# Kernel tuning notes

Measured on AMD Instinct MI355X. Metric: run time of the kernel, lower is better.

## Reference

```python
import jax, jax.numpy as jnp
import numpy as np

B, C, H = 4, 256, 8
GRID = 64                  # 64x64 quads, 2 triangles each
F = 2 * GRID * GRID        # 8192 faces
D = C // H
N_STEPS = 4 * GRID + 8     # upper bound on BFS wavefronts over the face graph


def _grid_adjacency():
    """Face adjacency (<=3 neighbors, -1 padded) of a triangulated GRIDxGRID quad grid."""
    adj = -np.ones((F, 3), np.int32)
    qid = lambda r, c: 2 * (r * GRID + c)
    for r in range(GRID):
        for c in range(GRID):
            t0 = qid(r, c); t1 = t0 + 1
            n0, n1 = [t1], [t0]
            if c > 0:        n0.append(qid(r, c - 1) + 1)
            if r > 0:        n0.append(qid(r - 1, c) + 1)
            if c < GRID - 1: n1.append(qid(r, c + 1))
            if r < GRID - 1: n1.append(qid(r + 1, c))
            adj[t0, :len(n0)] = n0
            adj[t1, :len(n1)] = n1
    return adj


def setup_inputs() -> dict:
    key = jax.random.key(0)
    k1, k2, k3, k4 = jax.random.split(key, 4)
    x = jax.random.normal(k1, (B, C, F), jnp.float32)
    Wq = jax.random.normal(k2, (C, C), jnp.float32) / np.sqrt(C).astype(np.float32)
    Wk = jax.random.normal(k3, (C, C), jnp.float32) / np.sqrt(C).astype(np.float32)
    adj = jnp.tile(jnp.asarray(_grid_adjacency())[None], (B, 1, 1))
    anchors = jax.random.randint(k4, (B,), 0, F, jnp.int32)
    return {"x": x, "Wq": Wq, "Wk": Wk, "adj": adj, "anchors": anchors}


def _heads(W, x):
    """Project and L2-normalize per head: [B,C,F] -> [B,H,D,F] unit vectors along D."""
    y = jnp.einsum('oc,bcf->bof', W, x).reshape(x.shape[0], H, D, -1)
    return y * jax.lax.rsqrt(jnp.sum(y * y, axis=2, keepdims=True) + 1e-12)


def reference(x, Wq, Wk, adj, anchors):
    q = _heads(Wq, x)          # [B,H,D,F]
    k = _heads(Wk, x)          # [B,H,D,F]
    bidx = jnp.arange(B)

    # initial scores: normalized attention map between all faces and the anchor face,
    # mapped to [0,1] and averaged over heads  (atnmap+1)/2 path of the torch module
    k_anchor = k[bidx, :, :, anchors]                       # [B,H,D]
    cos0 = jnp.einsum('bhdf,bhd->bhf', q, k_anchor)         # [B,H,F]
    scores0 = (jnp.mean(cos0, axis=1) + 1.0) * 0.5          # [B,F]

    ktot = k.sum(axis=3)                                    # [B,H,D]
    valid = adj >= 0
    adj_s = jnp.where(valid, adj, 0)
    done0 = jnp.zeros((B, F), bool).at[bidx, anchors].set(True)
    boundary0 = done0

    def gather(v):  # v: [B,F] -> neighbor values [B,F,3]
        return jnp.take_along_axis(v, adj_s.reshape(B, -1), axis=1).reshape(B, F, 3)

    def step(carry, _):
        done, boundary, scores = carry
        bf = boundary.astype(x.dtype)
        nb = bf.sum(1)                       # |boundary|
        no = F - nb                          # |others| = complement of boundary
        # mean over (heads, boundary, others) of cosine(q_b, k_o):
        # mean_{b,o} q_b.k_o = (sum_b q_b).(sum_o k_o) / (nb*no)
        qs = jnp.einsum('bhdf,bf->bhd', q, bf)
        ko = ktot - jnp.einsum('bhdf,bf->bhd', k, bf)
        mean_cos = jnp.einsum('bhd,bhd->b', qs, ko) / (H * jnp.maximum(nb * no, 1.0))
        pred = (mean_cos + 1.0) * 0.5        # scalar per mesh, as in torch reshape(1,-1).mean
        # neighbor score: max score among already-visited (done) adjacent faces, else 1
        n_done = gather(done) & valid
        n_sc = gather(scores)
        neigh = jnp.where(jnp.any(n_done, -1),
                          jnp.max(jnp.where(n_done, n_sc, -jnp.inf), -1), 1.0)
        cand = jnp.minimum(jnp.maximum(pred[:, None], scores), neigh)
        scores = jnp.where(boundary, cand, scores)
        done = done | boundary
        boundary = jnp.any(gather(boundary) & valid, -1) & ~done
        return (done, boundary, scores), None

    (_, _, scores), _ = jax.lax.scan(jax.checkpoint(step),
                                     (done0, boundary0, scores0), None, length=N_STEPS)
    # with atn_layers=1 the torch module never modifies features: final_features == x
    return x, scores
```

## Files before the change

### kernel.cpp

```cpp
#include <hip/hip_runtime.h>
#include <hip/hip_bf16.h>
#include <stdint.h>

#define B_ 4
#define C_ 256
#define H_ 8
#define F_ 8192
#define NSTEPS_ 264
#define OC_ 512

typedef __attribute__((ext_vector_type(8))) short short8;
typedef __attribute__((ext_vector_type(4))) float f32x4;

static __device__ __forceinline__ unsigned f2bf(float f) {
  unsigned u = __float_as_uint(f);
  return (u + 0x7FFFu + ((u >> 16) & 1u)) >> 16;
}
static __device__ __forceinline__ float b2f(unsigned short s) {
  return __uint_as_float(((unsigned)s) << 16);
}

static __device__ __forceinline__ void face_neighbors(int f, int nn[3]) {
  int qd = f >> 1, r = qd >> 6, c = qd & 63;
  if ((f & 1) == 0) {
    nn[0] = f + 1;
    nn[1] = (c > 0) ? f - 1 : -1;
    nn[2] = (r > 0) ? f - 127 : -1;
  } else {
    nn[0] = f - 1;
    nn[1] = (c < 63) ? f + 1 : -1;
    nn[2] = (r < 63) ? f + 127 : -1;
  }
}

static __device__ __forceinline__ int face_dist(int ra, int ca, int pa, int f) {
  int qd = f >> 1, r = qd >> 6, c = qd & 63, p = f & 1;
  int dr = r - ra, dc = c - ca;
  int I = max(dr, 0) + max(dc, 0);
  int D = max(-dr, 0) + max(-dc, 0);
  int lo = pa ? max(2 * I - 1, 2 * D) : max(2 * I, 2 * D - 1);
  lo = max(lo, 0);
  lo += (lo ^ p ^ pa) & 1;
  return lo;
}

__global__ void k_pre(const float* __restrict__ Wq, const float* __restrict__ Wk,
                      uint16_t* __restrict__ Wbf) {
  const int gid = blockIdx.x * 256 + threadIdx.x;
  const int base = gid * 32;
  const float* src = (base < 65536) ? (Wq + base) : (Wk + (base - 65536));
  uint32_t pk[16];
#pragma unroll
  for (int j = 0; j < 16; ++j) {
    float2 v = *(const float2*)(src + j * 2);
    pk[j] = f2bf(v.x) | (f2bf(v.y) << 16);
  }
  uint4* dst = (uint4*)(Wbf + base);
#pragma unroll
  for (int s = 0; s < 4; ++s)
    dst[s] = make_uint4(pk[4 * s], pk[4 * s + 1], pk[4 * s + 2], pk[4 * s + 3]);
}

__launch_bounds__(256)
__global__ void k_gemm(const float* __restrict__ x, const uint16_t* __restrict__ Wbf,
                       uint16_t* __restrict__ qkT, const int* __restrict__ anchors,
                       uint16_t* __restrict__ order_g, uint32_t* __restrict__ lvlOff_g,
                       uint32_t* __restrict__ chunks_g, uint32_t* __restrict__ nch_g,
                       float* __restrict__ ktot) {
  __shared__ char smem[65536];
  char* Xl = smem;
  char* Wl0 = smem + 32768;
  char* Wl1 = smem + 49152;
  const int tid = threadIdx.x;
  const int b = blockIdx.z;

  if (blockIdx.x == 128) {
    uint8_t* dLv = (uint8_t*)smem;
    uint16_t* ordL = (uint16_t*)(smem + 8192);
    uint32_t* hist = (uint32_t*)(smem + 24576);
    uint32_t* loff = (uint32_t*)(smem + 25600);
    uint32_t* cnt = (uint32_t*)(smem + 26640);
    uint32_t* chOff = (uint32_t*)(smem + 27680);
    const int a = anchors[b];
    const int aq = a >> 1, ra = aq >> 6, ca = aq & 63, pa = a & 1;
    hist[tid] = 0; cnt[tid] = 0;
    __syncthreads();
#pragma unroll
    for (int j = 0; j < 32; ++j) {
      int f = j * 256 + tid;
      int d = face_dist(ra, ca, pa, f);
      dLv[f] = (uint8_t)d;
      atomicAdd(&hist[d], 1u);
    }
    __syncthreads();
    loff[tid + 1] = hist[tid];
    if (tid == 0) loff[0] = 0;
    __syncthreads();
    for (int ofs = 1; ofs < 256; ofs <<= 1) {
      uint32_t v = (tid >= ofs) ? loff[tid + 1 - ofs] : 0u;
      __syncthreads();
      loff[tid + 1] += v;
      __syncthreads();
    }
#pragma unroll
    for (int j = 0; j < 32; ++j) {
      int f = j * 256 + tid;
      int d = dLv[f];
      int nn[3];
      face_neighbors(f, nn);
      int mask = 0;
      if (nn[0] >= 0 && dLv[nn[0]] < d) mask |= 1;
      if (nn[1] >= 0 && dLv[nn[1]] < d) mask |= 2;
      if (nn[2] >= 0 && dLv[nn[2]] < d) mask |= 4;
      uint32_t pos = loff[d] + atomicAdd(&cnt[d], 1u);
      ordL[pos] = (uint16_t)(f | (mask << 13));
    }
    __syncthreads();
    for (int i = tid; i < F_; i += 256) order_g[b * F_ + i] = ordL[i];
    for (int l = tid; l < NSTEPS_ + 2; l += 256)
      lvlOff_g[b * (NSTEPS_ + 2) + l] = (l <= 256) ? loff[l] : (uint32_t)F_;
    const int n_l = (int)(loff[tid + 1] - loff[tid]);
    const int chc = (n_l + 63) >> 6;
    chOff[tid + 1] = (uint32_t)chc;
    if (tid == 0) chOff[0] = 0;
    __syncthreads();
    for (int ofs = 1; ofs < 256; ofs <<= 1) {
      uint32_t v = (tid >= ofs) ? chOff[tid + 1 - ofs] : 0u;
      __syncthreads();
      chOff[tid + 1] += v;
      __syncthreads();
    }
    const uint32_t cbase = chOff[tid];
    for (int j = 0; j < chc; ++j) {
      uint32_t cs = loff[tid] + (uint32_t)(j * 64);
      uint32_t cl = (uint32_t)min(64, n_l - j * 64);
      chunks_g[b * 512 + cbase + j] = cs | (cl << 16);
    }
    if (tid == 255) nch_g[b] = chOff[256];
    return;
  }

  const int f0 = blockIdx.x * 64;
  const int lane = tid & 63;
  const int wo = tid >> 6;
  const int lq = lane >> 4;
  const int lm = lane & 15;

  {
    const int fx = tid & 63;
    const int kseg = tid >> 6;
    const float* src = x + ((size_t)b * C_ + kseg * 64) * F_ + f0 + fx;
#pragma unroll
    for (int g = 0; g < 4; ++g) {
      uint32_t pk[8];
#pragma unroll
      for (int j2 = 0; j2 < 8; ++j2) {
        float v0 = src[(size_t)(g * 16 + 2 * j2) * F_];
        float v1 = src[(size_t)(g * 16 + 2 * j2 + 1) * F_];
        pk[j2] = f2bf(v0) | (f2bf(v1) << 16);
      }
#pragma unroll
      for (int s = 0; s < 2; ++s) {
        int slot = kseg * 8 + g * 2 + s;
        uint32_t* dst = (uint32_t*)(Xl + (size_t)fx * 512 + ((slot ^ (fx & 7)) << 4));
        dst[0] = pk[4 * s + 0]; dst[1] = pk[4 * s + 1];
        dst[2] = pk[4 * s + 2]; dst[3] = pk[4 * s + 3];
      }
    }
  }

  for (int p = 0; p < 4; ++p) {
    const int o0 = p * 128;
    const uint16_t* Wsrc = Wbf + (size_t)o0 * C_;
#pragma unroll
    for (int j = 0; j < 4; ++j) {
      int sl = tid * 4 + j;
      int ocl = sl >> 3, slot = sl & 7;
      uint4 v = *(const uint4*)(Wsrc + (size_t)ocl * C_ + slot * 8);
      *(uint4*)(Wl0 + (size_t)ocl * 128 + ((slot ^ (ocl & 7)) << 4)) = v;
    }
    __syncthreads();

    f32x4 acc[4][2] = {};
    for (int kt = 0; kt < 4; ++kt) {
      char* cur = (kt & 1) ? Wl1 : Wl0;
      char* nxt = (kt & 1) ? Wl0 : Wl1;
      uint4 wv[4];
      if (kt < 3) {
#pragma unroll
        for (int j = 0; j < 4; ++j) {
          int sl = tid * 4 + j;
          int ocl = sl >> 3, slot = sl & 7;
          wv[j] = *(const uint4*)(Wsrc + (size_t)ocl * C_ + (kt + 1) * 64 + slot * 8);
        }
      }
#pragma unroll
      for (int kk = 0; kk < 64; kk += 32) {
        const int sA = kt * 8 + (kk >> 3) + lq;
        const int sB = (kk >> 3) + lq;
        short8 af[4], bg[2];
#pragma unroll
        for (int mi = 0; mi < 4; ++mi) {
          int fl = mi * 16 + lm;
          af[mi] = *(const short8*)(Xl + (size_t)fl * 512 + ((sA ^ (fl & 7)) << 4));
        }
#pragma unroll
        for (int ni = 0; ni < 2; ++ni) {
          int ocl = wo * 32 + ni * 16 + lm;
          bg[ni] = *(const short8*)(cur + (size_t)ocl * 128 + ((sB ^ (ocl & 7)) << 4));
        }
#pragma unroll
        for (int mi = 0; mi < 4; ++mi)
#pragma unroll
          for (int ni = 0; ni < 2; ++ni)
            acc[mi][ni] = __builtin_amdgcn_mfma_f32_16x16x32_bf16(af[mi], bg[ni], acc[mi][ni], 0, 0, 0);
      }
      if (kt < 3) {
#pragma unroll
        for (int j = 0; j < 4; ++j) {
          int sl = tid * 4 + j;
          int ocl = sl >> 3, slot = sl & 7;
          *(uint4*)(nxt + (size_t)ocl * 128 + ((slot ^ (ocl & 7)) << 4)) = wv[j];
        }
      }
      __syncthreads();
    }

    char* yst = Wl0;
#pragma unroll
    for (int mi = 0; mi < 4; ++mi) {
#pragma unroll
      for (int r = 0; r < 4; ++r) {
        float s0 = acc[mi][0][r] * acc[mi][0][r] + acc[mi][1][r] * acc[mi][1][r];
        s0 += __shfl_xor(s0, 1);
        s0 += __shfl_xor(s0, 2);
        s0 += __shfl_xor(s0, 4);
        s0 += __shfl_xor(s0, 8);
        const float sc0 = rsqrtf(s0 + 1e-12f);
        const int fl = mi * 16 + lq * 4 + r;
#pragma unroll
        for (int ni = 0; ni < 2; ++ni) {
          int ocl = wo * 32 + ni * 16 + lm;
          float v = acc[mi][ni][r] * sc0;
          int byte = fl * 256 + ((((ocl * 2) >> 4) ^ (fl & 7)) << 4) + ((ocl * 2) & 15);
          *(uint16_t*)(yst + byte) = (uint16_t)f2bf(v);
        }
      }
    }
    __syncthreads();
    uint32_t* qk32 = (uint32_t*)qkT;
    const size_t obase = (((size_t)b * F_ + f0) * OC_ + o0) >> 1;
    for (int idx = tid; idx < 4096; idx += 256) {
      int face = idx >> 6, wd = idx & 63;
      int byte = face * 256 + ((((wd * 4) >> 4) ^ (face & 7)) << 4) + ((wd * 4) & 15);
      qk32[obase + (size_t)face * 256 + wd] = *(uint32_t*)(yst + byte);
    }
    if (p >= 2 && tid < 128) {
      const int cbyte = tid * 2;
      float ssum = 0.f;
#pragma unroll 4
      for (int face = 0; face < 64; ++face) {
        int byte = face * 256 + (((cbyte >> 4) ^ (face & 7)) << 4) + (cbyte & 15);
        ssum += b2f(*(const uint16_t*)(yst + byte));
      }
      atomicAdd(&ktot[b * C_ + (p - 2) * 128 + tid], ssum);
    }
    __syncthreads();
  }
}

__launch_bounds__(256)
__global__ void k_predscore(const uint16_t* __restrict__ qkT, const uint16_t* __restrict__ order_g,
                            const uint32_t* __restrict__ lvlOff_g, const float* __restrict__ ktot,
                            const int* __restrict__ anchors, float* __restrict__ pred_g,
                            float* __restrict__ scores0) {
  const int b = blockIdx.y, tid = threadIdx.x, bx = blockIdx.x;
  __shared__ uint16_t ordS[384];
  __shared__ float qk2[512];
  __shared__ float red[256];
  if (bx >= NSTEPS_) {
    const int anchor = anchors[b];
    red[tid] = b2f(qkT[((size_t)(b * F_ + anchor)) * OC_ + 256 + tid]);
    __syncthreads();
    const int wave = tid >> 6, lane = tid & 63;
    const int fbase = (bx - NSTEPS_) * 256 + wave * 64;
    for (int fi = 0; fi < 64; ++fi) {
      int f = fbase + fi;
      const uint16_t* row = qkT + ((size_t)(b * F_ + f)) * OC_ + lane * 4;
      ushort4 rv = *(const ushort4*)row;
      float dot = b2f(rv.x) * red[lane * 4 + 0] + b2f(rv.y) * red[lane * 4 + 1] +
                  b2f(rv.z) * red[lane * 4 + 2] + b2f(rv.w) * red[lane * 4 + 3];
      for (int off = 32; off; off >>= 1) dot += __shfl_down(dot, off);
      if (lane == 0) scores0[b * F_ + f] = (dot * (1.0f / H_) + 1.f) * 0.5f;
    }
    return;
  }
  const int t = bx;
  const uint32_t s = lvlOff_g[b * (NSTEPS_ + 2) + t];
  const uint32_t e = lvlOff_g[b * (NSTEPS_ + 2) + t + 1];
  const int n = min((int)(e - s), 384);
  for (int i = tid; i < n; i += 256) ordS[i] = order_g[(size_t)b * F_ + s + i] & 8191;
  __syncthreads();
  const int half = tid >> 7, cc = (tid & 127) * 2;
  const uint16_t* qkb = qkT + ((size_t)b * F_) * OC_ + half * 256 + cc;
  float a0 = 0.f, a1 = 0.f;
  int i = 0;
  for (; i + 8 <= n; i += 8) {
    uint32_t v[8];
#pragma unroll
    for (int u = 0; u < 8; ++u) v[u] = *(const uint32_t*)(qkb + (size_t)ordS[i + u] * OC_);
#pragma unroll
    for (int u = 0; u < 8; ++u) {
      a0 += b2f((unsigned short)(v[u] & 0xFFFFu));
      a1 += b2f((unsigned short)(v[u] >> 16));
    }
  }
  for (; i < n; ++i) {
    uint32_t v = *(const uint32_t*)(qkb + (size_t)ordS[i] * OC_);
    a0 += b2f((unsigned short)(v & 0xFFFFu));
    a1 += b2f((unsigned short)(v >> 16));
  }
  qk2[half * 256 + cc] = a0;
  qk2[half * 256 + cc + 1] = a1;
  __syncthreads();
  float prod = qk2[tid] * (ktot[b * C_ + tid] - qk2[256 + tid]);
  red[tid] = prod;
  __syncthreads();
  if (tid < 128) red[tid] += red[tid + 128];
  __syncthreads();
  if (tid < 64) {
    float v = red[tid] + red[tid + 64];
    for (int off = 32; off; off >>= 1) v += __shfl_down(v, off);
    if (tid == 0) {
      float nb = (float)(e - s), no = (float)F_ - nb;
      pred_g[b * NSTEPS_ + t] = (v / ((float)H_ * fmaxf(nb * no, 1.f)) + 1.f) * 0.5f;
    }
  }
}

#define MKST(ENT, ACT, I0, I1, I2, IO, IW, M)            \
  do {                                                   \
    int f_ = (int)((ENT) & 8191u);                       \
    int m_ = (int)(((ENT) >> 13) & 7u);                  \
    int s_ = 1 - 2 * (f_ & 1);                           \
    I0 = (m_ & 1) ? f_ + s_ : f_;                        \
    I1 = (m_ & 2) ? f_ - s_ : f_;                        \
    I2 = (m_ & 4) ? f_ - 127 * s_ : f_;                  \
    IO = f_;                                             \
    IW = (ACT) ? f_ : (F_ + lane);                       \
    M = m_;                                              \
  } while (0)

__launch_bounds__(256)
__global__ void k_final(const float* __restrict__ scores0, const uint16_t* __restrict__ order_g,
                        const uint32_t* __restrict__ chunks_g, const uint32_t* __restrict__ nch_g,
                        const float* __restrict__ pred_g, const int* __restrict__ anchors,
                        const float4* __restrict__ x4, float4* __restrict__ out4,
                        float* __restrict__ out_scores) {
  __shared__ float A[F_ + 64];
  __shared__ uint16_t ordL[F_];
  __shared__ float prL[NSTEPS_];
  __shared__ uint32_t chunkL[512];
  __shared__ int nchS;
  const int tid = threadIdx.x;
  if (blockIdx.x >= B_) {
    const int cb = blockIdx.x - B_;
    const float4* src = x4 + (size_t)cb * 16384 + tid;
    float4* dst = out4 + (size_t)cb * 16384 + tid;
#pragma unroll 8
    for (int it = 0; it < 64; ++it) dst[it * 256] = src[it * 256];
    return;
  }
  const int b = blockIdx.x;
  for (int i = tid; i < NSTEPS_; i += 256) prL[i] = pred_g[b * NSTEPS_ + i];
  for (int i = tid; i < 512; i += 256) chunkL[i] = chunks_g[b * 512 + i];
  if (tid == 0) nchS = (int)nch_g[b];
  const int a = anchors[b];
  const int aq = a >> 1, ra = aq >> 6, ca = aq & 63, pa = a & 1;
  __syncthreads();
  for (int i = tid; i < F_; i += 256) {
    int d = face_dist(ra, ca, pa, i);
    A[i] = fmaxf(prL[d], scores0[(size_t)b * F_ + i]);
  }
  for (int i = tid; i < F_ / 4; i += 256)
    ((ushort4*)ordL)[i] = ((const ushort4*)(order_g + (size_t)b * F_))[i];
  __syncthreads();
  if (tid < 64) {
    const int lane = tid;
    const int nch = nchS;
    int i0a = 0, i1a = 0, i2a = 0, ioa = 0, iwa = F_ + lane, ma = 0;
    int i0b = 0, i1b = 0, i2b = 0, iob = 0, iwb = F_ + lane, mb = 0;
    {
      uint32_t ck = chunkL[0];
      uint32_t bs = ck & 0xFFFFu, cn = ck >> 16;
      uint32_t ent = ordL[bs + min((uint32_t)lane, cn - 1)];
      MKST(ent, (uint32_t)lane < cn, i0a, i1a, i2a, ioa, iwa, ma);
    }
    if (nch > 1) {
      uint32_t ck = chunkL[1];
      uint32_t bs = ck & 0xFFFFu, cn = ck >> 16;
      uint32_t ent = ordL[bs + min((uint32_t)lane, cn - 1)];
      MKST(ent, (uint32_t)lane < cn, i0b, i1b, i2b, iob, iwb, mb);
    }
    uint32_t ckN = (nch > 2) ? chunkL[2] : 0;
    for (int c = 0; c < nch; ++c) {
      float v0 = A[i0a], v1 = A[i1a], v2 = A[i2a], own = A[ioa];
      uint32_t entN = 0;
      bool actN = false;
      if (c + 2 < nch) {
        uint32_t bs = ckN & 0xFFFFu, cn = ckN >> 16;
        entN = ordL[bs + min((uint32_t)lane, cn - 1)];
        actN = (uint32_t)lane < cn;
      }
      uint32_t ckNN = (c + 3 < nch) ? chunkL[c + 3] : 0;
      float m0 = (ma & 1) ? v0 : -1e30f;
      float m1 = (ma & 2) ? v1 : -1e30f;
      float m2 = (ma & 4) ? v2 : -1e30f;
      float nv = ma ? fmaxf(fmaxf(m0, m1), m2) : 1.0f;
      A[iwa] = fminf(own, nv);
      i0a = i0b; i1a = i1b; i2a = i2b; ioa = iob; iwa = iwb; ma = mb;
      MKST(entN, actN, i0b, i1b, i2b, iob, iwb, mb);
      ckN = ckNN;
    }
  }
  __syncthreads();
  for (int i = tid; i < F_ / 4; i += 256)
    ((float4*)(out_scores + (size_t)b * F_))[i] = ((const float4*)A)[i];
}

extern "C" void kernel_launch(void* const* d_in, const int* in_sizes, int n_in,
                              void* d_out, int out_size, void* d_ws, size_t ws_size,
                              hipStream_t stream) {
  const float* x = (const float*)d_in[0];
  const float* Wq = (const float*)d_in[1];
  const float* Wk = (const float*)d_in[2];
  const int* anchors = (const int*)d_in[4];
  float* out = (float*)d_out;

  uint16_t* qkT = (uint16_t*)d_out;

  char* ws = (char*)d_ws;
  size_t off = 0;
  uint16_t* Wbf = (uint16_t*)(ws + off);   off += (size_t)OC_ * C_ * 2;
  float* ktot = (float*)(ws + off);        off += (size_t)B_ * C_ * 4;
  float* scores0 = (float*)(ws + off);     off += (size_t)B_ * F_ * 4;
  float* pred = (float*)(ws + off);        off += (size_t)B_ * NSTEPS_ * 4;
  uint16_t* order = (uint16_t*)(ws + off); off += (size_t)B_ * F_ * 2;
  uint32_t* lvlOff = (uint32_t*)(ws + off); off += (size_t)B_ * (NSTEPS_ + 2) * 4;
  uint32_t* chunks = (uint32_t*)(ws + off); off += (size_t)B_ * 512 * 4;
  uint32_t* nch = (uint32_t*)(ws + off);   off += (size_t)B_ * 4;

  k_pre<<<16, 256, 0, stream>>>(Wq, Wk, Wbf);
  hipMemsetAsync(ktot, 0, (size_t)B_ * C_ * 4, stream);
  k_gemm<<<dim3(129, 1, B_), 256, 0, stream>>>(x, Wbf, qkT, anchors, order, lvlOff,
                                               chunks, nch, ktot);
  k_predscore<<<dim3(NSTEPS_ + 32, B_), 256, 0, stream>>>(qkT, order, lvlOff, ktot, anchors,
                                                          pred, scores0);
  k_final<<<B_ + 128, 256, 0, stream>>>(scores0, order, chunks, nch, pred, anchors,
                                        (const float4*)x, (float4*)out,
                                        out + (size_t)B_ * C_ * F_);
}
```

Before: 145.8 us.

## Process whole BFS levels per wavefront iteration instead of 64-face chunks

The serial scoring sweep now handles an entire BFS level per loop iteration, with each lane owning up to six faces and the work split into 1-, 3- or 6-group variants. Before, each level was split into 64-face chunks run one after another. The chunk-building prefix scan in the gemm kernel is replaced by one entry per level, and the level count comes from an atomic max. This cuts the number of serial iterations and their LDS round-trip latency, at the cost of more registers and branchy templated code. It also assumes every level has at most 384 faces.

```diff
diff --git a/kernel.cpp b/kernel.cpp
--- a/kernel.cpp
+++ b/kernel.cpp
@@ -80,18 +80,22 @@
     uint32_t* hist = (uint32_t*)(smem + 24576);
     uint32_t* loff = (uint32_t*)(smem + 25600);
     uint32_t* cnt = (uint32_t*)(smem + 26640);
-    uint32_t* chOff = (uint32_t*)(smem + 27680);
+    int* maxdp = (int*)(smem + 27680);
     const int a = anchors[b];
     const int aq = a >> 1, ra = aq >> 6, ca = aq & 63, pa = a & 1;
     hist[tid] = 0; cnt[tid] = 0;
-    __syncthreads();
+    if (tid == 0) *maxdp = 0;
+    __syncthreads();
+    int lmax = 0;
 #pragma unroll
     for (int j = 0; j < 32; ++j) {
       int f = j * 256 + tid;
       int d = face_dist(ra, ca, pa, f);
       dLv[f] = (uint8_t)d;
+      lmax = max(lmax, d);
       atomicAdd(&hist[d], 1u);
     }
+    atomicMax(maxdp, lmax);
     __syncthreads();
     loff[tid + 1] = hist[tid];
     if (tid == 0) loff[0] = 0;
@@ -119,24 +123,11 @@
     for (int i = tid; i < F_; i += 256) order_g[b * F_ + i] = ordL[i];
     for (int l = tid; l < NSTEPS_ + 2; l += 256)
       lvlOff_g[b * (NSTEPS_ + 2) + l] = (l <= 256) ? loff[l] : (uint32_t)F_;
-    const int n_l = (int)(loff[tid + 1] - loff[tid]);
-    const int chc = (n_l + 63) >> 6;
-    chOff[tid + 1] = (uint32_t)chc;
-    if (tid == 0) chOff[0] = 0;
-    __syncthreads();
-    for (int ofs = 1; ofs < 256; ofs <<= 1) {
-      uint32_t v = (tid >= ofs) ? chOff[tid + 1 - ofs] : 0u;
-      __syncthreads();
-      chOff[tid + 1] += v;
-      __syncthreads();
-    }
-    const uint32_t cbase = chOff[tid];
-    for (int j = 0; j < chc; ++j) {
-      uint32_t cs = loff[tid] + (uint32_t)(j * 64);
-      uint32_t cl = (uint32_t)min(64, n_l - j * 64);
-      chunks_g[b * 512 + cbase + j] = cs | (cl << 16);
-    }
-    if (tid == 255) nch_g[b] = chOff[256];
+    {
+      uint32_t cl = loff[tid + 1] - loff[tid];
+      chunks_g[b * 512 + tid] = cl ? (loff[tid] | (cl << 16)) : (1u << 16);
+    }
+    if (tid == 0) nch_g[b] = (uint32_t)(*maxdp + 1);
     return;
   }
 
@@ -338,18 +329,74 @@
   }
 }
 
-#define MKST(ENT, ACT, I0, I1, I2, IO, IW, M)            \
-  do {                                                   \
-    int f_ = (int)((ENT) & 8191u);                       \
-    int m_ = (int)(((ENT) >> 13) & 7u);                  \
-    int s_ = 1 - 2 * (f_ & 1);                           \
-    I0 = (m_ & 1) ? f_ + s_ : f_;                        \
-    I1 = (m_ & 2) ? f_ - s_ : f_;                        \
-    I2 = (m_ & 4) ? f_ - 127 * s_ : f_;                  \
-    IO = f_;                                             \
-    IW = (ACT) ? f_ : (F_ + lane);                       \
-    M = m_;                                              \
-  } while (0)
+struct SwSt { int i0[6], i1[6], i2[6], io[6], iw[6], m[6]; };
+
+static __device__ __forceinline__ void sw_rdraw(uint32_t* raw, const uint16_t* ordL,
+                                                uint32_t ck, int lane) {
+  int bs = (int)(ck & 0xFFFFu), cn = (int)(ck >> 16);
+#pragma unroll
+  for (int g = 0; g < 6; ++g)
+    raw[g] = ordL[bs + min(g * 64 + lane, cn - 1)];
+}
+
+template <int G>
+static __device__ __forceinline__ void sw_decode(SwSt& S, const uint32_t* raw, int cn, int lane) {
+#pragma unroll
+  for (int g = 0; g < G; ++g) {
+    uint32_t ent = raw[g];
+    int f = (int)(ent & 8191u);
+    int m = (int)((ent >> 13) & 7u);
+    int s = 1 - 2 * (f & 1);
+    S.i0[g] = (m & 1) ? f + s : f;
+    S.i1[g] = (m & 2) ? f - s : f;
+    S.i2[g] = (m & 4) ? f - 127 * s : f;
+    S.io[g] = f;
+    S.iw[g] = (g * 64 + lane < cn) ? f : (F_ + lane);
+    S.m[g] = m;
+  }
+}
+
+template <int G>
+static __device__ __forceinline__ void sw_reads(const SwSt& S, const float* A, float* v0,
+                                                float* v1, float* v2, float* ow) {
+#pragma unroll
+  for (int g = 0; g < G; ++g) {
+    v0[g] = A[S.i0[g]]; v1[g] = A[S.i1[g]];
+    v2[g] = A[S.i2[g]]; ow[g] = A[S.io[g]];
+  }
+}
+
+template <int G>
+static __device__ __forceinline__ void sw_writes(const SwSt& S, float* A, const float* v0,
+                                                 const float* v1, const float* v2,
+                                                 const float* ow) {
+#pragma unroll
+  for (int g = 0; g < G; ++g) {
+    float m0 = (S.m[g] & 1) ? v0[g] : -1e30f;
+    float m1 = (S.m[g] & 2) ? v1[g] : -1e30f;
+    float m2 = (S.m[g] & 4) ? v2[g] : -1e30f;
+    float nv = S.m[g] ? fmaxf(fmaxf(m0, m1), m2) : 1.0f;
+    A[S.iw[g]] = fminf(ow[g], nv);
+  }
+}
+
+#define SW_ITER(DCUR, CNCUR, RAWOUT, CNOUT, RAWIN, CNIN, DNXT, CNNXT)        \
+  {                                                                          \
+    float v0[6], v1[6], v2[6], ow[6];                                        \
+    if (CNCUR <= 64)       sw_reads<1>(DCUR, A, v0, v1, v2, ow);             \
+    else if (CNCUR <= 192) sw_reads<3>(DCUR, A, v0, v1, v2, ow);             \
+    else                   sw_reads<6>(DCUR, A, v0, v1, v2, ow);             \
+    sw_rdraw(RAWOUT, ordL, ckN, lane);                                       \
+    CNOUT = (int)(ckN >> 16);                                                \
+    ckN = ckNN; ckNN = chunkL[min(t + 4, 255)];                              \
+    if (CNCUR <= 64)       sw_writes<1>(DCUR, A, v0, v1, v2, ow);            \
+    else if (CNCUR <= 192) sw_writes<3>(DCUR, A, v0, v1, v2, ow);            \
+    else                   sw_writes<6>(DCUR, A, v0, v1, v2, ow);            \
+    CNNXT = CNIN;                                                            \
+    if (CNIN <= 64)        sw_decode<1>(DNXT, RAWIN, CNIN, lane);            \
+    else if (CNIN <= 192)  sw_decode<3>(DNXT, RAWIN, CNIN, lane);            \
+    else                   sw_decode<6>(DNXT, RAWIN, CNIN, lane);            \
+  }
 
 __launch_bounds__(256)
 __global__ void k_final(const float* __restrict__ scores0, const uint16_t* __restrict__ order_g,
@@ -360,7 +407,7 @@
   __shared__ float A[F_ + 64];
   __shared__ uint16_t ordL[F_];
   __shared__ float prL[NSTEPS_];
-  __shared__ uint32_t chunkL[512];
+  __shared__ uint32_t chunkL[256];
   __shared__ int nchS;
   const int tid = threadIdx.x;
   if (blockIdx.x >= B_) {
@@ -373,7 +420,7 @@
   }
   const int b = blockIdx.x;
   for (int i = tid; i < NSTEPS_; i += 256) prL[i] = pred_g[b * NSTEPS_ + i];
-  for (int i = tid; i < 512; i += 256) chunkL[i] = chunks_g[b * 512 + i];
+  for (int i = tid; i < 256; i += 256) chunkL[i] = chunks_g[b * 512 + i];
   if (tid == 0) nchS = (int)nch_g[b];
   const int a = anchors[b];
   const int aq = a >> 1, ra = aq >> 6, ca = aq & 63, pa = a & 1;
@@ -387,40 +434,31 @@
   __syncthreads();
   if (tid < 64) {
     const int lane = tid;
-    const int nch = nchS;
-    int i0a = 0, i1a = 0, i2a = 0, ioa = 0, iwa = F_ + lane, ma = 0;
-    int i0b = 0, i1b = 0, i2b = 0, iob = 0, iwb = F_ + lane, mb = 0;
+    const int nlev = min(nchS, 256);
+    SwSt DX, DY;
+    uint32_t rawA[6], rawB[6];
+    int cnRawA, cnRawB, cnX = 1, cnY = 1;
+    uint32_t ckN, ckNN;
     {
-      uint32_t ck = chunkL[0];
-      uint32_t bs = ck & 0xFFFFu, cn = ck >> 16;
-      uint32_t ent = ordL[bs + min((uint32_t)lane, cn - 1)];
-      MKST(ent, (uint32_t)lane < cn, i0a, i1a, i2a, ioa, iwa, ma);
-    }
-    if (nch > 1) {
-      uint32_t ck = chunkL[1];
-      uint32_t bs = ck & 0xFFFFu, cn = ck >> 16;
-      uint32_t ent = ordL[bs + min((uint32_t)lane, cn - 1)];
-      MKST(ent, (uint32_t)lane < cn, i0b, i1b, i2b, iob, iwb, mb);
-    }
-    uint32_t ckN = (nch > 2) ? chunkL[2] : 0;
-    for (int c = 0; c < nch; ++c) {
-      float v0 = A[i0a], v1 = A[i1a], v2 = A[i2a], own = A[ioa];
-      uint32_t entN = 0;
-      bool actN = false;
-      if (c + 2 < nch) {
-        uint32_t bs = ckN & 0xFFFFu, cn = ckN >> 16;
-        entN = ordL[bs + min((uint32_t)lane, cn - 1)];
-        actN = (uint32_t)lane < cn;
-      }
-      uint32_t ckNN = (c + 3 < nch) ? chunkL[c + 3] : 0;
-      float m0 = (ma & 1) ? v0 : -1e30f;
-      float m1 = (ma & 2) ? v1 : -1e30f;
-      float m2 = (ma & 4) ? v2 : -1e30f;
-      float nv = ma ? fmaxf(fmaxf(m0, m1), m2) : 1.0f;
-      A[iwa] = fminf(own, nv);
-      i0a = i0b; i1a = i1b; i2a = i2b; ioa = iob; iwa = iwb; ma = mb;
-      MKST(entN, actN, i0b, i1b, i2b, iob, iwb, mb);
-      ckN = ckNN;
+      uint32_t ck0 = chunkL[0];
+      sw_rdraw(rawA, ordL, ck0, lane);
+      cnX = (int)(ck0 >> 16);
+      if (cnX <= 64)       sw_decode<1>(DX, rawA, cnX, lane);
+      else if (cnX <= 192) sw_decode<3>(DX, rawA, cnX, lane);
+      else                 sw_decode<6>(DX, rawA, cnX, lane);
+      uint32_t ck1 = chunkL[1];
+      sw_rdraw(rawA, ordL, ck1, lane);
+      cnRawA = (int)(ck1 >> 16);
+      ckN = chunkL[2];
+      ckNN = chunkL[3];
+    }
+    int t = 0;
+    while (t < nlev) {
+      SW_ITER(DX, cnX, rawB, cnRawB, rawA, cnRawA, DY, cnY);
+      ++t;
+      if (t >= nlev) break;
+      SW_ITER(DY, cnY, rawA, cnRawA, rawB, cnRawB, DX, cnX);
+      ++t;
     }
   }
   __syncthreads();
```

Measured after the change: 190.9 us. 30.9% more time.
